# Optimization experiments

Measured on AMD Instinct MI355X. Metric: run time of the kernel, lower is better.

Reference implementation:

```python
import jax, jax.numpy as jnp
import numpy as np
from jax import lax

B, C, IMG, PATCH = 128, 3, 224, 16
EMB, HEADS = 384, 6
NPATCH = (IMG // PATCH) ** 2          # 196
NTOK = NPATCH + 1                     # 197 (cls token)
HID = int(EMB * 4.0)                  # 1536 (also expert hidden)
NE, K = 4, 2                          # num_experts (hardcoded 4), top-k
NCLS = 1000


def _ln(x, g, b, eps=1e-5):
    m = jnp.mean(x, axis=-1, keepdims=True)
    v = jnp.mean((x - m) ** 2, axis=-1, keepdims=True)
    return (x - m) * lax.rsqrt(v + eps) * g + b


def setup_inputs() -> dict:
    key = jax.random.key(0)
    ks = jax.random.split(key, 16)
    s = 0.02
    return {
        "x": jax.random.normal(ks[0], (B, C, IMG, IMG), jnp.float32),
        "conv_w": jax.random.normal(ks[1], (EMB, C, PATCH, PATCH), jnp.float32) * s,
        "conv_b": jnp.zeros((EMB,), jnp.float32),
        "cls_token": jax.random.normal(ks[2], (1, 1, EMB), jnp.float32) * s,
        "pos_embed": jax.random.normal(ks[3], (1, NTOK, EMB), jnp.float32) * s,
        "ln1_g": jnp.ones((EMB,), jnp.float32),
        "ln1_b": jnp.zeros((EMB,), jnp.float32),
        "in_proj_w": jax.random.normal(ks[4], (3 * EMB, EMB), jnp.float32) * s,
        "in_proj_b": jnp.zeros((3 * EMB,), jnp.float32),
        "out_proj_w": jax.random.normal(ks[5], (EMB, EMB), jnp.float32) * s,
        "out_proj_b": jnp.zeros((EMB,), jnp.float32),
        "router_w": jax.random.normal(ks[6], (NE, EMB), jnp.float32) * s,
        "router_b": jnp.zeros((NE,), jnp.float32),
        "ew1": jax.random.normal(ks[7], (NE, EMB, HID), jnp.float32) * s,
        "eb1": jnp.zeros((NE, HID), jnp.float32),
        "ew2": jax.random.normal(ks[8], (NE, HID, EMB), jnp.float32) * s,
        "eb2": jnp.zeros((NE, EMB), jnp.float32),
        "ln2_g": jnp.ones((EMB,), jnp.float32),
        "ln2_b": jnp.zeros((EMB,), jnp.float32),
        "head_w": jax.random.normal(ks[9], (NCLS, EMB), jnp.float32) * s,
        "head_b": jnp.zeros((NCLS,), jnp.float32),
    }


def reference(x, conv_w, conv_b, cls_token, pos_embed,
              ln1_g, ln1_b, in_proj_w, in_proj_b, out_proj_w, out_proj_b,
              router_w, router_b, ew1, eb1, ew2, eb2,
              ln2_g, ln2_b, head_w, head_b):
    # ---- patch embedding: Conv2d(stride=kernel=patch) -> [B, N, E]
    h = lax.conv_general_dilated(x, conv_w, window_strides=(PATCH, PATCH),
                                 padding="VALID",
                                 dimension_numbers=("NCHW", "OIHW", "NCHW"))
    h = h + conv_b[None, :, None, None]
    h = h.reshape(B, EMB, NPATCH).transpose(0, 2, 1)          # [B, 196, E]
    h = jnp.concatenate([jnp.broadcast_to(cls_token, (B, 1, EMB)), h], axis=1)
    h = h + pos_embed                                         # [B, 197, E]

    # ---- SelfAttentionBlock (NOTE: no residual; same LN applied twice, as in source)
    hn = _ln(h, ln1_g, ln1_b)
    qkv = hn @ in_proj_w.T + in_proj_b                        # [B, N, 3E]
    q, k, v = jnp.split(qkv, 3, axis=-1)
    hd = EMB // HEADS
    q = q.reshape(B, NTOK, HEADS, hd)
    k = k.reshape(B, NTOK, HEADS, hd)
    v = v.reshape(B, NTOK, HEADS, hd)
    att = jnp.einsum("bqhd,bkhd->bhqk", q, k) / np.sqrt(hd).astype(np.float32)
    att = jax.nn.softmax(att, axis=-1)
    o = jnp.einsum("bhqk,bkhd->bqhd", att, v).reshape(B, NTOK, EMB)
    o = o @ out_proj_w.T + out_proj_b
    h = _ln(o, ln1_g, ln1_b)                                  # second LN, same params

    # ---- MoE: dense all-expert FFN + top-k gather + mean
    scores = jax.nn.softmax(h @ router_w.T + router_b, axis=-1)   # [B, N, NE]
    topk_vals, topk_idx = lax.top_k(scores, K)                    # [B, N, K]
    flat = h.reshape(B * NTOK, EMB)
    eh = jax.nn.gelu(jnp.einsum("te,neh->tnh", flat, ew1) + eb1, approximate=False)
    eo = jnp.einsum("tnh,nhe->tne", eh, ew2) + eb2                # [BN, NE, E]
    idx = topk_idx.reshape(B * NTOK, K, 1)
    sel = jnp.take_along_axis(eo, idx, axis=1)                    # [BN, K, E]
    h = sel.mean(axis=1).reshape(B, NTOK, EMB)

    # ---- final norm + classification head on cls token
    h = _ln(h, ln2_g, ln2_b)
    return h[:, 0] @ head_w.T + head_b                            # [B, NCLS]
```

## Files before the change

kernel.cpp:

```cpp
#include <hip/hip_runtime.h>
#include <cstdint>
#include <cstddef>

typedef _Float16 f16;
typedef _Float16 f16x2 __attribute__((ext_vector_type(2)));
typedef _Float16 f16x8 __attribute__((ext_vector_type(8)));
typedef float    f32x4 __attribute__((ext_vector_type(4)));

constexpr int NTOKC  = 197;
constexpr int TTOK   = 128 * 197;
constexpr int EMB    = 384;
constexpr int HID    = 1536;

constexpr size_t OFF_CONVW   = 0;
constexpr size_t OFF_EW1T    = 1179648;
constexpr size_t OFF_EW2T    = 5898240;
constexpr size_t OFF_HEADW16 = 10616832;
constexpr size_t OFF_XCLS16  = 11403264;
constexpr size_t OFF_Q       = 11404800;
constexpr size_t OFF_HCLS16  = 11799552;
constexpr size_t OFF_MASKW   = 11897856;
constexpr size_t OFF_EH      = 11899904;
constexpr size_t OFF_EPART   = 13472768;
constexpr size_t OFF_HFIN    = 16618496;
constexpr size_t OFF_XH      = 16716800;
constexpr size_t OFF_R       = 36082688;
constexpr size_t OFF_CVEC    = 36094976;
constexpr size_t OFF_U16     = 36099072;
constexpr size_t OFF_O16     = 36688896;
constexpr size_t OFF_WV16    = 36787200;
constexpr size_t OFF_WOUT16  = 37082112;
constexpr size_t OFF_O2CLS   = 37377024;
constexpr size_t OFF_P32     = 37573632;
constexpr size_t OFF_SG      = 38212608;
constexpr size_t OFF_SCLS    = 38817792;
constexpr size_t WS_NEEDED   = 38818816;

__device__ __forceinline__ void gload16(const void* g, void* l) {
  __builtin_amdgcn_global_load_lds(
      (__attribute__((address_space(1))) void*)(void*)g,
      (__attribute__((address_space(3))) void*)l, 16, 0, 0);
}

__global__ __launch_bounds__(256) void prep_cast_k(
    const float* __restrict__ conv_w, const float* __restrict__ head_w,
    const float* __restrict__ inp_w, const float* __restrict__ outp_w,
    f16* __restrict__ convw, f16* __restrict__ headw16,
    f16* __restrict__ wv16, f16* __restrict__ wout16) {
  int i = blockIdx.x * 256 + threadIdx.x;
  if (i < 294912) convw[i] = (f16)conv_w[i];
  int j = i - 294912;
  if (j >= 0 && j < 393216) {
    int row = j / 384;
    headw16[j] = (row < 1000) ? (f16)head_w[j] : (f16)0.f;
  }
  int k = i - 688128;
  if (k >= 0 && k < 147456) wv16[k] = (f16)inp_w[294912 + k];
  int l = i - 835584;
  if (l >= 0 && l < 147456) wout16[l] = (f16)outp_w[l];
}

__global__ __launch_bounds__(256) void transpose_cast_k(
    const float* __restrict__ in, f16* __restrict__ outp, int R, int C) {
  __shared__ float tile[32][33];
  int e = blockIdx.z;
  const float* pin = in + (size_t)e * R * C;
  f16* pout = outp + (size_t)e * R * C;
  int c0 = blockIdx.x * 32, r0 = blockIdx.y * 32;
  int tx = threadIdx.x & 31, ty = threadIdx.x >> 5;
#pragma unroll
  for (int i = 0; i < 4; i++)
    tile[ty + 8 * i][tx] = pin[(size_t)(r0 + ty + 8 * i) * C + c0 + tx];
  __syncthreads();
#pragma unroll
  for (int i = 0; i < 4; i++)
    pout[(size_t)(c0 + ty + 8 * i) * R + r0 + tx] = (f16)tile[tx][ty + 8 * i];
}

__global__ __launch_bounds__(384) void clsprep_k(
    const float* __restrict__ cls, const float* __restrict__ posw,
    const float* __restrict__ g, const float* __restrict__ bb,
    const float* __restrict__ Wq, const float* __restrict__ bq,
    f16* __restrict__ xcls16, float* __restrict__ qout) {
  __shared__ float xs[EMB];
  __shared__ float red[16];
  int t = threadIdx.x, lane = t & 63, wave = t >> 6;
  float v = cls[t] + posw[t];
  float s = v, sq = v * v;
#pragma unroll
  for (int off = 32; off; off >>= 1) {
    s += __shfl_xor(s, off);
    sq += __shfl_xor(sq, off);
  }
  if (lane == 0) { red[wave] = s; red[8 + wave] = sq; }
  __syncthreads();
  float S = 0.f, SQ = 0.f;
#pragma unroll
  for (int i = 0; i < 6; i++) { S += red[i]; SQ += red[8 + i]; }
  float m = S * (1.f / 384.f);
  float rs = rsqrtf(SQ * (1.f / 384.f) - m * m + 1e-5f);
  float y = (v - m) * rs * g[t] + bb[t];
  xs[t] = y;
  xcls16[t] = (f16)y;
  __syncthreads();
  const float4* w4 = (const float4*)(Wq + (size_t)t * EMB);
  const float4* s4 = (const float4*)xs;
  float a = bq[t];
#pragma unroll 8
  for (int i = 0; i < 96; i++) {
    float4 xx = s4[i], ww = w4[i];
    a += xx.x * ww.x + xx.y * ww.y + xx.z * ww.z + xx.w * ww.w;
  }
  qout[t] = a;
}

__global__ __launch_bounds__(384) void rprep_k(
    const float* __restrict__ inp_w, const float* __restrict__ inp_b,
    const float* __restrict__ qv, const f16* __restrict__ xcls16,
    float* __restrict__ Rg, float* __restrict__ Cg, float* __restrict__ Scls) {
  int h = blockIdx.x, t = threadIdx.x;
  __shared__ float qs[64];
  __shared__ float cred[64];
  __shared__ float sred[6];
  if (t < 64) {
    float q = qv[h * 64 + t];
    qs[t] = q;
    cred[t] = q * inp_b[384 + h * 64 + t];
  }
  __syncthreads();
  const float* wp = inp_w + ((size_t)(384 + h * 64)) * 384 + t;
  float a = 0.f;
#pragma unroll 8
  for (int d = 0; d < 64; d++) a += wp[(size_t)d * 384] * qs[d];
  Rg[h * 384 + t] = a;
  float part = a * (float)xcls16[t];
  int lane = t & 63, wave = t >> 6;
#pragma unroll
  for (int off = 32; off; off >>= 1) part += __shfl_xor(part, off);
  if (lane == 0) sred[wave] = part;
  __syncthreads();
  if (t == 0) {
    float c = 0.f;
    for (int d = 0; d < 64; d++) c += cred[d];
    Cg[h] = c;
    float stot = c;
#pragma unroll
    for (int i = 0; i < 6; i++) stot += sred[i];
    Scls[h] = stot;
  }
}

__global__ __launch_bounds__(384) void bcast_cls_k(
    const f16* __restrict__ xcls16, const float* __restrict__ Scls,
    f16* __restrict__ xh, float* __restrict__ Sg) {
  int b = blockIdx.x, t = threadIdx.x;
  xh[(size_t)b * NTOKC * EMB + t] = xcls16[t];
  if (t < 6) Sg[((size_t)b * 6 + t) * 197] = Scls[t];
}

__global__ __launch_bounds__(1024) void embed_ln_k(
    const float* __restrict__ img, const f16* __restrict__ B,
    const float* __restrict__ bias, const float* __restrict__ posw,
    const float* __restrict__ g, const float* __restrict__ bb,
    const float* __restrict__ Rg, const float* __restrict__ Cg,
    f16* __restrict__ xh, float* __restrict__ Sg) {
  __shared__ __attribute__((aligned(16))) char smem[57344];
  f16* As0 = (f16*)smem;
  f16* As1 = (f16*)(smem + 4096);
  f16* Bs0 = (f16*)(smem + 8192);
  f16* Bs1 = (f16*)(smem + 32768);
  const int K = 768;
  const int NT = 24;
  const int tid = threadIdx.x;
  const int lane = tid & 63;
  const int wave = tid >> 6;
  const int rowgrp = wave & 3;
  const int colgrp = wave >> 2;
  const int m0 = (int)blockIdx.x * 64;
  const int fr = lane & 15;
  const int fq = lane >> 4;

  f32x4 acc[6];
#pragma unroll
  for (int j = 0; j < 6; j++) acc[j] = f32x4{0.f, 0.f, 0.f, 0.f};

  const int sr = lane >> 2, sc = (lane & 3) * 8;
  const float* abase = nullptr;
  int adoff = 0;
  if (wave < 4) {
    int row = m0 + wave * 16 + sr;
    int bimg = row / 196;
    int pp = row - bimg * 196;
    int py = pp / 14, px = pp - py * 14;
    int kx0 = sc & 15;
    abase = img + ((size_t)(bimg * 3) * 224 + py * 16) * 224 + px * 16 + kx0;
    adoff = (wave * 16 + sr) * 32 + sc;
  }
  const f16* gb0 = nullptr;
  int lboff = 0;
  if (wave >= 4) {
    int brow = (wave - 4) * 32;
    gb0 = B + (size_t)(brow + sr) * K + sc;
    lboff = brow * 32;
  }

  float4 n0, n1;
  if (wave < 4) {
    {
      int col = sc;
      const float* src = abase + (col >> 8) * 50176 + ((col >> 4) & 15) * 224;
      float4 p0 = *(const float4*)src;
      float4 p1 = *(const float4*)(src + 4);
      f16x8 hv;
      hv[0] = (f16)p0.x; hv[1] = (f16)p0.y; hv[2] = (f16)p0.z; hv[3] = (f16)p0.w;
      hv[4] = (f16)p1.x; hv[5] = (f16)p1.y; hv[6] = (f16)p1.z; hv[7] = (f16)p1.w;
      *(f16x8*)(As0 + adoff) = hv;
    }
    {
      int col = 32 + sc;
      const float* src = abase + (col >> 8) * 50176 + ((col >> 4) & 15) * 224;
      n0 = *(const float4*)src;
      n1 = *(const float4*)(src + 4);
    }
  } else {
    gload16(gb0, Bs0 + lboff);
    gload16(gb0 + (size_t)16 * K, Bs0 + lboff + 16 * 32);
    gb0 += 32;
  }
  __syncthreads();

  f16* AsC = As0; f16* AsN = As1;
  f16* BsC = Bs0; f16* BsN = Bs1;

  for (int t = 0; t < NT; ++t) {
    if (wave < 4) {
      if (t + 1 < NT) {
        f16x8 hv;
        hv[0] = (f16)n0.x; hv[1] = (f16)n0.y; hv[2] = (f16)n0.z; hv[3] = (f16)n0.w;
        hv[4] = (f16)n1.x; hv[5] = (f16)n1.y; hv[6] = (f16)n1.z; hv[7] = (f16)n1.w;
        *(f16x8*)(AsN + adoff) = hv;
      }
      if (t + 2 < NT) {
        int col = (t + 2) * 32 + sc;
        const float* src = abase + (col >> 8) * 50176 + ((col >> 4) & 15) * 224;
        n0 = *(const float4*)src;
        n1 = *(const float4*)(src + 4);
      }
    } else {
      if (t + 1 < NT) {
        gload16(gb0, BsN + lboff);
        gload16(gb0 + (size_t)16 * K, BsN + lboff + 16 * 32);
        gb0 += 32;
      }
    }
    f16x8 af = *(const f16x8*)&AsC[(rowgrp * 16 + fr) * 32 + fq * 8];
#pragma unroll
    for (int j = 0; j < 6; j++) {
      f16x8 bf = *(const f16x8*)&BsC[(colgrp * 96 + j * 16 + fr) * 32 + fq * 8];
      acc[j] = __builtin_amdgcn_mfma_f32_16x16x32_f16(af, bf, acc[j], 0, 0, 0);
    }
    __syncthreads();
    f16* tA = AsC; AsC = AsN; AsN = tA;
    f16* tB = BsC; BsC = BsN; BsN = tB;
  }

  float* prm   = (float*)smem;
  float* psum  = (float*)(smem + 4608);
  float* pqsum = (float*)(smem + 5632);
  float* Rs2   = (float*)(smem + 6656);
  float* psc   = (float*)(smem + 15872);
  for (int i = tid; i < 1152; i += 1024)
    prm[i] = (i < 384) ? bias[i] : ((i < 768) ? g[i - 384] : bb[i - 768]);
  for (int i = tid; i < 2304; i += 1024) Rs2[i] = Rg[i];
  __syncthreads();

  float v[4][6];
#pragma unroll
  for (int rg = 0; rg < 4; rg++) {
    int lrow = rowgrp * 16 + fq * 4 + rg;
    int row = m0 + lrow;
    int bimg = row / 196;
    int pp = row - bimg * 196;
    const float* prow = posw + (size_t)(pp + 1) * EMB;
    float s = 0.f, sq = 0.f;
#pragma unroll
    for (int j = 0; j < 6; j++) {
      int col = colgrp * 96 + j * 16 + fr;
      float t = acc[j][rg] + prm[col] + prow[col];
      v[rg][j] = t;
      s += t; sq += t * t;
    }
#pragma unroll
    for (int off = 1; off < 16; off <<= 1) {
      s += __shfl_xor(s, off);
      sq += __shfl_xor(sq, off);
    }
    if (fr == 0) { psum[lrow * 4 + colgrp] = s; pqsum[lrow * 4 + colgrp] = sq; }
  }
  __syncthreads();

#pragma unroll
  for (int rg = 0; rg < 4; rg++) {
    int lrow = rowgrp * 16 + fq * 4 + rg;
    float S = psum[lrow * 4] + psum[lrow * 4 + 1] + psum[lrow * 4 + 2] + psum[lrow * 4 + 3];
    float SQ = pqsum[lrow * 4] + pqsum[lrow * 4 + 1] + pqsum[lrow * 4 + 2] + pqsum[lrow * 4 + 3];
    float m = S * (1.f / 384.f);
    float rs = rsqrtf(SQ * (1.f / 384.f) - m * m + 1e-5f);
    int row = m0 + lrow;
    int bimg = row / 196;
    int pp = row - bimg * 196;
    f16* orow = xh + ((size_t)bimg * NTOKC + pp + 1) * EMB;
#pragma unroll
    for (int j = 0; j < 6; j++) {
      int col = colgrp * 96 + j * 16 + fr;
      float y = (v[rg][j] - m) * rs * prm[384 + col] + prm[768 + col];
      v[rg][j] = y;
      orow[col] = (f16)y;
    }
  }

#pragma unroll
  for (int h = 0; h < 6; h++) {
    float rv[6];
#pragma unroll
    for (int j = 0; j < 6; j++)
      rv[j] = Rs2[h * 384 + colgrp * 96 + j * 16 + fr];
#pragma unroll
    for (int rg = 0; rg < 4; rg++) {
      float p = v[rg][0] * rv[0] + v[rg][1] * rv[1] + v[rg][2] * rv[2]
              + v[rg][3] * rv[3] + v[rg][4] * rv[4] + v[rg][5] * rv[5];
#pragma unroll
      for (int off = 1; off < 16; off <<= 1) p += __shfl_xor(p, off);
      if (fr == 0) psc[(rowgrp * 16 + fq * 4 + rg) * 24 + colgrp * 6 + h] = p;
    }
  }
  __syncthreads();
  if (tid < 384) {
    int lrow = tid / 6, h = tid - lrow * 6;
    float s = psc[lrow * 24 + h] + psc[lrow * 24 + 6 + h]
            + psc[lrow * 24 + 12 + h] + psc[lrow * 24 + 18 + h] + Cg[h];
    int row = m0 + lrow;
    int bimg = row / 196, pp = row - bimg * 196;
    Sg[((size_t)bimg * 6 + h) * 197 + pp + 1] = s;
  }
}

__global__ __launch_bounds__(384) void softmax_k(
    const float* __restrict__ Sg, float* __restrict__ P32) {
  const int b = blockIdx.x, tid = threadIdx.x;
  const int wave = tid >> 6, lane = tid & 63;
  const float* sp = Sg + ((size_t)b * 6 + wave) * 197;
  float z[4], pk[4];
#pragma unroll
  for (int k = 0; k < 4; k++) {
    int t = lane + 64 * k;
    z[k] = (t < 197) ? sp[t] * 0.125f : -1e30f;
    pk[k] = 0.f;
  }
  float mx = fmaxf(fmaxf(z[0], z[1]), fmaxf(z[2], z[3]));
#pragma unroll
  for (int off = 32; off; off >>= 1) mx = fmaxf(mx, __shfl_xor(mx, off));
  float sum = 0.f;
#pragma unroll
  for (int k = 0; k < 4; k++) {
    int t = lane + 64 * k;
    if (t < 197) {
      pk[k] = __expf(z[k] - mx);
      sum += pk[k];
    }
  }
#pragma unroll
  for (int off = 32; off; off >>= 1) sum += __shfl_xor(sum, off);
  float si = 1.f / sum;
#pragma unroll
  for (int k = 0; k < 4; k++) {
    int t = lane + 64 * k;
    if (t < 208) P32[(size_t)b * 1248 + wave * 208 + t] = pk[k] * si;
  }
}

__global__ __launch_bounds__(256) void u_gemv_k(
    const float* __restrict__ P32, const f16* __restrict__ xh,
    f16* __restrict__ U16) {
  __shared__ float pf[6 * 208];
  __shared__ float part[4][64][12];
  const int cq = (int)blockIdx.x;
  const int b  = (int)blockIdx.y;
  const int tid = threadIdx.x;
  for (int i = tid; i < 1248; i += 256) pf[i] = P32[(size_t)b * 1248 + i];
  __syncthreads();
  const int cp = tid & 63;
  const int tq = tid >> 6;
  const int col0 = cq * 128 + cp * 2;
  const int t0 = 49 * tq;
  const int t1 = (tq == 3) ? 197 : t0 + 49;
  float acc[12];
#pragma unroll
  for (int r = 0; r < 12; r++) acc[r] = 0.f;
  const f16* xp = xh + ((size_t)b * NTOKC + t0) * EMB + col0;
#pragma unroll 2
  for (int t = t0; t < t1; t++) {
    f16x2 xv = *(const f16x2*)xp;
    float x0 = (float)xv[0];
    float x1 = (float)xv[1];
    xp += EMB;
#pragma unroll
    for (int h = 0; h < 6; h++) {
      float p = pf[h * 208 + t];
      acc[h * 2]     += p * x0;
      acc[h * 2 + 1] += p * x1;
    }
  }
#pragma unroll
  for (int r = 0; r < 12; r++) part[tq][cp][r] = acc[r];
  __syncthreads();
#pragma unroll
  for (int k = 0; k < 3; k++) {
    int idx = tid + k * 256;
    int cp2 = idx / 12, slot = idx - cp2 * 12;
    int h = slot >> 1, c01 = slot & 1;
    float u = part[0][cp2][slot] + part[1][cp2][slot] +
              part[2][cp2][slot] + part[3][cp2][slot];
    U16[(size_t)b * 2304 + h * 384 + cq * 128 + cp2 * 2 + c01] = (f16)u;
  }
}

__global__ __launch_bounds__(256) void vproj_k(
    const f16* __restrict__ U16, const f16* __restrict__ wv16,
    const float* __restrict__ inp_b, f16* __restrict__ O16) {
  __shared__ f16 As[128 * 32];
  __shared__ f16 Bs[64 * 32];
  const int tid = threadIdx.x;
  const int lane = tid & 63;
  const int wave = tid >> 6;
  const int h = (int)blockIdx.x;
  const int wm = (wave >> 1) * 64;
  const int wn = (wave & 1) * 32;
  const int fr = lane & 15;
  const int fq = lane >> 4;
  const float* bv = inp_b + 768 + h * 64;

  f32x4 acc[4][2];
#pragma unroll
  for (int i = 0; i < 4; i++)
#pragma unroll
    for (int j = 0; j < 2; j++) acc[i][j] = f32x4{0.f, 0.f, 0.f, 0.f};

  const int sr = lane >> 2;
  const int sc = (lane & 3) * 8;
  const f16* ag = U16 + (size_t)(wave * 32 + sr) * 2304 + h * 384 + sc;
  const f16* bg = wv16 + (size_t)(h * 64 + wave * 16 + sr) * 384 + sc;
  const size_t rstepA = (size_t)16 * 2304;
  f16* la = As + wave * 32 * 32;
  f16* lb = Bs + wave * 16 * 32;

  for (int k0 = 0; k0 < 384; k0 += 32) {
    gload16(ag, la);  gload16(ag + rstepA, la + 16 * 32);
    gload16(bg, lb);
    ag += 32; bg += 32;
    __syncthreads();
    f16x8 af[4], bf[2];
#pragma unroll
    for (int i = 0; i < 4; i++)
      af[i] = *(const f16x8*)&As[(wm + i * 16 + fr) * 32 + fq * 8];
#pragma unroll
    for (int j = 0; j < 2; j++)
      bf[j] = *(const f16x8*)&Bs[(wn + j * 16 + fr) * 32 + fq * 8];
#pragma unroll
    for (int i = 0; i < 4; i++)
#pragma unroll
      for (int j = 0; j < 2; j++)
        acc[i][j] = __builtin_amdgcn_mfma_f32_16x16x32_f16(af[i], bf[j], acc[i][j], 0, 0, 0);
    __syncthreads();
  }

#pragma unroll
  for (int i = 0; i < 4; i++)
#pragma unroll
    for (int j = 0; j < 2; j++)
#pragma unroll
      for (int rg = 0; rg < 4; rg++) {
        int gm = wm + i * 16 + fq * 4 + rg;
        int gn = wn + j * 16 + fr;
        O16[(size_t)gm * EMB + h * 64 + gn] = (f16)(acc[i][j][rg] + bv[gn]);
      }
}

__global__ __launch_bounds__(256) void oproj_k(
    const f16* __restrict__ O16, const f16* __restrict__ wout16,
    const float* __restrict__ bout, float* __restrict__ o2cls) {
  __shared__ f16 As[128 * 32];
  __shared__ f16 Bs[64 * 32];
  const int tid = threadIdx.x;
  const int lane = tid & 63;
  const int wave = tid >> 6;
  const int n0 = (int)blockIdx.x * 64;
  const int wm = (wave >> 1) * 64;
  const int wn = (wave & 1) * 32;
  const int fr = lane & 15;
  const int fq = lane >> 4;

  f32x4 acc[4][2];
#pragma unroll
  for (int i = 0; i < 4; i++)
#pragma unroll
    for (int j = 0; j < 2; j++) acc[i][j] = f32x4{0.f, 0.f, 0.f, 0.f};

  const int sr = lane >> 2;
  const int sc = (lane & 3) * 8;
  const f16* ag = O16 + (size_t)(wave * 32 + sr) * 384 + sc;
  const f16* bg = wout16 + (size_t)(n0 + wave * 16 + sr) * 384 + sc;
  const size_t rstep = (size_t)16 * 384;
  f16* la = As + wave * 32 * 32;
  f16* lb = Bs + wave * 16 * 32;

  for (int k0 = 0; k0 < 384; k0 += 32) {
    gload16(ag, la);  gload16(ag + rstep, la + 16 * 32);
    gload16(bg, lb);
    ag += 32; bg += 32;
    __syncthreads();
    f16x8 af[4], bf[2];
#pragma unroll
    for (int i = 0; i < 4; i++)
      af[i] = *(const f16x8*)&As[(wm + i * 16 + fr) * 32 + fq * 8];
#pragma unroll
    for (int j = 0; j < 2; j++)
      bf[j] = *(const f16x8*)&Bs[(wn + j * 16 + fr) * 32 + fq * 8];
#pragma unroll
    for (int i = 0; i < 4; i++)
#pragma unroll
      for (int j = 0; j < 2; j++)
        acc[i][j] = __builtin_amdgcn_mfma_f32_16x16x32_f16(af[i], bf[j], acc[i][j], 0, 0, 0);
    __syncthreads();
  }

#pragma unroll
  for (int i = 0; i < 4; i++)
#pragma unroll
    for (int j = 0; j < 2; j++)
#pragma unroll
      for (int rg = 0; rg < 4; rg++) {
        int gm = wm + i * 16 + fq * 4 + rg;
        int gn = n0 + wn + j * 16 + fr;
        o2cls[(size_t)gm * EMB + gn] = acc[i][j][rg] + bout[gn];
      }
}

__global__ __launch_bounds__(384) void ln_router_k(
    const float* __restrict__ o2cls, const float* __restrict__ g, const float* __restrict__ bb,
    const float* __restrict__ rw, const float* __restrict__ rb,
    f16* __restrict__ hcls16, float* __restrict__ maskw) {
  __shared__ float red[16];
  __shared__ float part[6][4];
  __shared__ float logits[4];
  int b = blockIdx.x, t = threadIdx.x;
  int lane = t & 63, wave = t >> 6;
  float v = o2cls[(size_t)b * EMB + t];
  float s = v, sq = v * v;
#pragma unroll
  for (int off = 32; off; off >>= 1) {
    s += __shfl_xor(s, off);
    sq += __shfl_xor(sq, off);
  }
  if (lane == 0) { red[wave] = s; red[8 + wave] = sq; }
  __syncthreads();
  float S = 0.f, SQ = 0.f;
#pragma unroll
  for (int i = 0; i < 6; i++) { S += red[i]; SQ += red[8 + i]; }
  float m = S * (1.f / 384.f);
  float rs = rsqrtf(SQ * (1.f / 384.f) - m * m + 1e-5f);
  float y = (v - m) * rs * g[t] + bb[t];
  hcls16[(size_t)b * EMB + t] = (f16)y;
  float p0 = y * rw[t];
  float p1 = y * rw[EMB + t];
  float p2 = y * rw[2 * EMB + t];
  float p3 = y * rw[3 * EMB + t];
#pragma unroll
  for (int off = 32; off; off >>= 1) {
    p0 += __shfl_xor(p0, off);
    p1 += __shfl_xor(p1, off);
    p2 += __shfl_xor(p2, off);
    p3 += __shfl_xor(p3, off);
  }
  if (lane == 0) { part[wave][0] = p0; part[wave][1] = p1; part[wave][2] = p2; part[wave][3] = p3; }
  __syncthreads();
  if (t < 4) {
    float a = rb[t];
#pragma unroll
    for (int i = 0; i < 6; i++) a += part[i][t];
    logits[t] = a;
  }
  __syncthreads();
  if (t == 0) {
    float l0 = logits[0], l1 = logits[1], l2 = logits[2], l3 = logits[3];
    int i1 = 0; float b1 = l0;
    if (l1 > b1) { b1 = l1; i1 = 1; }
    if (l2 > b1) { b1 = l2; i1 = 2; }
    if (l3 > b1) { b1 = l3; i1 = 3; }
    int i2 = -1; float b2 = 0.f;
    float lv[4] = {l0, l1, l2, l3};
#pragma unroll
    for (int i = 0; i < 4; i++) {
      if (i == i1) continue;
      if (i2 < 0 || lv[i] > b2) { i2 = i; b2 = lv[i]; }
    }
#pragma unroll
    for (int e = 0; e < 4; e++)
      maskw[(size_t)b * 4 + e] = (e == i1 || e == i2) ? 0.5f : 0.f;
  }
}

__global__ __launch_bounds__(256) void moe1_k(
    const f16* __restrict__ A, const f16* __restrict__ Bm,
    const float* __restrict__ bias, f16* __restrict__ outh) {
  __shared__ f16 As[128 * 32];
  __shared__ f16 Bs[64 * 32];
  const int K = EMB;
  const int tid = threadIdx.x;
  const int lane = tid & 63;
  const int wave = tid >> 6;
  const int e = (int)blockIdx.y;
  const int n0 = (int)blockIdx.x * 64;
  const int wm = (wave >> 1) * 64;
  const int wn = (wave & 1) * 32;
  const int fr = lane & 15;
  const int fq = lane >> 4;
  Bm += (size_t)e * HID * EMB;
  bias += (size_t)e * HID;

  f32x4 acc[4][2];
#pragma unroll
  for (int i = 0; i < 4; i++)
#pragma unroll
    for (int j = 0; j < 2; j++) acc[i][j] = f32x4{0.f, 0.f, 0.f, 0.f};

  const int sr = lane >> 2;
  const int sc = (lane & 3) * 8;
  const f16* ag = A + (size_t)(wave * 32 + sr) * K + sc;
  const f16* bg = Bm + (size_t)(n0 + wave * 16 + sr) * K + sc;
  const size_t rstep = (size_t)16 * K;
// ... 145 lines not shown
  const int wn = (wave & 1) * 64;
  const int fr = lane & 15;
  const int fq = lane >> 4;

  f32x4 acc[4][4];
#pragma unroll
  for (int i = 0; i < 4; i++)
#pragma unroll
    for (int j = 0; j < 4; j++) acc[i][j] = f32x4{0.f, 0.f, 0.f, 0.f};

  const int srow = wave * 32 + (lane >> 2);
  const int scol = (lane & 3) * 8;
  const f16* ag = A + (size_t)srow * K + scol;
  const f16* bg = B + (size_t)(n0 + srow) * K + scol;
  const size_t rstep = (size_t)16 * K;
  f16* la = As + wave * 32 * 32;
  f16* lb = Bs + wave * 32 * 32;

  for (int k0 = 0; k0 < K; k0 += 32) {
    gload16(ag, la);          gload16(ag + rstep, la + 16 * 32);
    gload16(bg, lb);          gload16(bg + rstep, lb + 16 * 32);
    ag += 32; bg += 32;
    __syncthreads();
    f16x8 af[4], bf[4];
#pragma unroll
    for (int i = 0; i < 4; i++) {
      af[i] = *(const f16x8*)&As[(wm + i * 16 + fr) * 32 + fq * 8];
      bf[i] = *(const f16x8*)&Bs[(wn + i * 16 + fr) * 32 + fq * 8];
    }
#pragma unroll
    for (int i = 0; i < 4; i++)
#pragma unroll
      for (int j = 0; j < 4; j++)
        acc[i][j] = __builtin_amdgcn_mfma_f32_16x16x32_f16(af[i], bf[j], acc[i][j], 0, 0, 0);
    __syncthreads();
  }

#pragma unroll
  for (int i = 0; i < 4; i++)
#pragma unroll
    for (int j = 0; j < 4; j++)
#pragma unroll
      for (int rg = 0; rg < 4; rg++) {
        int gm = wm + i * 16 + fq * 4 + rg;
        int gn = n0 + wn + j * 16 + fr;
        if (gn < 1000)
          outp[(size_t)gm * 1000 + gn] = acc[i][j][rg] + hb[gn];
      }
}

extern "C" void kernel_launch(void* const* d_in, const int* in_sizes, int n_in,
                              void* d_out, int out_size, void* d_ws, size_t ws_size,
                              hipStream_t stream) {
  const float* x      = (const float*)d_in[0];
  const float* conv_w = (const float*)d_in[1];
  const float* conv_b = (const float*)d_in[2];
  const float* cls_t  = (const float*)d_in[3];
  const float* pos    = (const float*)d_in[4];
  const float* ln1_g  = (const float*)d_in[5];
  const float* ln1_b  = (const float*)d_in[6];
  const float* inp_w  = (const float*)d_in[7];
  const float* inp_b  = (const float*)d_in[8];
  const float* outp_w = (const float*)d_in[9];
  const float* outp_b = (const float*)d_in[10];
  const float* rt_w   = (const float*)d_in[11];
  const float* rt_b   = (const float*)d_in[12];
  const float* ew1    = (const float*)d_in[13];
  const float* eb1    = (const float*)d_in[14];
  const float* ew2    = (const float*)d_in[15];
  const float* eb2    = (const float*)d_in[16];
  const float* ln2_g  = (const float*)d_in[17];
  const float* ln2_b  = (const float*)d_in[18];
  const float* head_w = (const float*)d_in[19];
  const float* head_b = (const float*)d_in[20];
  float* out = (float*)d_out;
  char* w = (char*)d_ws;
  if (ws_size < WS_NEEDED) return;

  f16* convw    = (f16*)(w + OFF_CONVW);
  f16* ew1t     = (f16*)(w + OFF_EW1T);
  f16* ew2t     = (f16*)(w + OFF_EW2T);
  f16* headw16  = (f16*)(w + OFF_HEADW16);
  f16* xcls16   = (f16*)(w + OFF_XCLS16);
  float* qvec   = (float*)(w + OFF_Q);
  f16* hcls16   = (f16*)(w + OFF_HCLS16);
  float* maskw  = (float*)(w + OFF_MASKW);
  f16* ehbuf    = (f16*)(w + OFF_EH);
  float* epart  = (float*)(w + OFF_EPART);
  f16* hfin     = (f16*)(w + OFF_HFIN);
  f16* xh       = (f16*)(w + OFF_XH);
  float* Rg     = (float*)(w + OFF_R);
  float* Cg     = (float*)(w + OFF_CVEC);
  f16* u16      = (f16*)(w + OFF_U16);
  f16* o16      = (f16*)(w + OFF_O16);
  f16* wv16     = (f16*)(w + OFF_WV16);
  f16* wout16   = (f16*)(w + OFF_WOUT16);
  float* o2cls  = (float*)(w + OFF_O2CLS);
  float* p32    = (float*)(w + OFF_P32);
  float* sg     = (float*)(w + OFF_SG);
  float* scls   = (float*)(w + OFF_SCLS);

  prep_cast_k<<<dim3(3840), 256, 0, stream>>>(
      conv_w, head_w, inp_w, outp_w, convw, headw16, wv16, wout16);
  transpose_cast_k<<<dim3(48, 12, 4), 256, 0, stream>>>(ew1, ew1t, 384, 1536);
  transpose_cast_k<<<dim3(12, 48, 4), 256, 0, stream>>>(ew2, ew2t, 1536, 384);

  clsprep_k<<<dim3(1), 384, 0, stream>>>(cls_t, pos, ln1_g, ln1_b, inp_w, inp_b, xcls16, qvec);
  rprep_k<<<dim3(6), 384, 0, stream>>>(inp_w, inp_b, qvec, xcls16, Rg, Cg, scls);
  bcast_cls_k<<<dim3(128), 384, 0, stream>>>(xcls16, scls, xh, sg);

  embed_ln_k<<<dim3(392), 1024, 0, stream>>>(
      x, convw, conv_b, pos, ln1_g, ln1_b, Rg, Cg, xh, sg);

  softmax_k<<<dim3(128), 384, 0, stream>>>(sg, p32);
  u_gemv_k<<<dim3(3, 128), 256, 0, stream>>>(p32, xh, u16);
  vproj_k<<<dim3(6), 256, 0, stream>>>(u16, wv16, inp_b, o16);
  oproj_k<<<dim3(6), 256, 0, stream>>>(o16, wout16, outp_b, o2cls);
  ln_router_k<<<dim3(128), 384, 0, stream>>>(
      o2cls, ln1_g, ln1_b, rt_w, rt_b, hcls16, maskw);

  moe1_k<<<dim3(24, 4), 256, 0, stream>>>(hcls16, ew1t, eb1, ehbuf);
  moe2_k<<<dim3(6, 4, 4), 256, 0, stream>>>(ehbuf, ew2t, epart);
  combine_ln2_k<<<dim3(128), 384, 0, stream>>>(epart, eb2, maskw, ln2_g, ln2_b, hfin);

  head_gemm_k<<<dim3(8), 256, 0, stream>>>(hfin, headw16, head_b, out);
  (void)in_sizes; (void)n_in; (void)out_size;
}
```

Baseline: 321.7 us.

## Fold V and output projections into one weight, merge prep kernels, swizzle LDS

Precomputes a fused matrix F = Wout·Wv per head, plus a combined bias, in a single merged prep kernel, so the V projection and output projection collapse into one split-K GEMM whose partial sums are reduced inside the LN/router kernel. The separate prep, transpose, cls-prep, broadcast and softmax kernels are folded into fewer launches, with softmax moved into u_gemv and the cls broadcast into embed_ln. The embedding GEMM gains an XOR-swizzled LDS layout and a deeper A-prefetch. This cuts launch count and intermediate buffers, at the cost of a larger fused-weight GEMM with a K of 2304 and extra prep work to build F.

```diff
diff --git a/kernel.cpp b/kernel.cpp
--- a/kernel.cpp
+++ b/kernel.cpp
@@ -17,7 +17,6 @@
 constexpr size_t OFF_EW2T    = 5898240;
 constexpr size_t OFF_HEADW16 = 10616832;
 constexpr size_t OFF_XCLS16  = 11403264;
-constexpr size_t OFF_Q       = 11404800;
 constexpr size_t OFF_HCLS16  = 11799552;
 constexpr size_t OFF_MASKW   = 11897856;
 constexpr size_t OFF_EH      = 11899904;
@@ -27,14 +26,12 @@
 constexpr size_t OFF_R       = 36082688;
 constexpr size_t OFF_CVEC    = 36094976;
 constexpr size_t OFF_U16     = 36099072;
-constexpr size_t OFF_O16     = 36688896;
-constexpr size_t OFF_WV16    = 36787200;
-constexpr size_t OFF_WOUT16  = 37082112;
-constexpr size_t OFF_O2CLS   = 37377024;
-constexpr size_t OFF_P32     = 37573632;
 constexpr size_t OFF_SG      = 38212608;
 constexpr size_t OFF_SCLS    = 38817792;
-constexpr size_t WS_NEEDED   = 38818816;
+constexpr size_t OFF_F       = 38818816;
+constexpr size_t OFF_B2      = 40588288;
+constexpr size_t OFF_FPART   = 40589824;
+constexpr size_t WS_NEEDED   = 41179648;
 
 __device__ __forceinline__ void gload16(const void* g, void* l) {
   __builtin_amdgcn_global_load_lds(
@@ -42,49 +39,101 @@
       (__attribute__((address_space(3))) void*)l, 16, 0, 0);
 }
 
-__global__ __launch_bounds__(256) void prep_cast_k(
+#define PACK8(hv, p0, p1) { hv[0]=(f16)p0.x; hv[1]=(f16)p0.y; hv[2]=(f16)p0.z; hv[3]=(f16)p0.w; \
+                            hv[4]=(f16)p1.x; hv[5]=(f16)p1.y; hv[6]=(f16)p1.z; hv[7]=(f16)p1.w; }
+
+__global__ __launch_bounds__(256) void prep_all_k(
     const float* __restrict__ conv_w, const float* __restrict__ head_w,
-    const float* __restrict__ inp_w, const float* __restrict__ outp_w,
+    const float* __restrict__ ew1, const float* __restrict__ ew2,
+    const float* __restrict__ inp_w, const float* __restrict__ inp_b,
+    const float* __restrict__ outp_w, const float* __restrict__ outp_b,
     f16* __restrict__ convw, f16* __restrict__ headw16,
-    f16* __restrict__ wv16, f16* __restrict__ wout16) {
-  int i = blockIdx.x * 256 + threadIdx.x;
-  if (i < 294912) convw[i] = (f16)conv_w[i];
-  int j = i - 294912;
-  if (j >= 0 && j < 393216) {
-    int row = j / 384;
-    headw16[j] = (row < 1000) ? (f16)head_w[j] : (f16)0.f;
-  }
-  int k = i - 688128;
-  if (k >= 0 && k < 147456) wv16[k] = (f16)inp_w[294912 + k];
-  int l = i - 835584;
-  if (l >= 0 && l < 147456) wout16[l] = (f16)outp_w[l];
-}
-
-__global__ __launch_bounds__(256) void transpose_cast_k(
-    const float* __restrict__ in, f16* __restrict__ outp, int R, int C) {
-  __shared__ float tile[32][33];
-  int e = blockIdx.z;
-  const float* pin = in + (size_t)e * R * C;
-  f16* pout = outp + (size_t)e * R * C;
-  int c0 = blockIdx.x * 32, r0 = blockIdx.y * 32;
-  int tx = threadIdx.x & 31, ty = threadIdx.x >> 5;
-#pragma unroll
-  for (int i = 0; i < 4; i++)
-    tile[ty + 8 * i][tx] = pin[(size_t)(r0 + ty + 8 * i) * C + c0 + tx];
-  __syncthreads();
-#pragma unroll
-  for (int i = 0; i < 4; i++)
-    pout[(size_t)(c0 + ty + 8 * i) * R + r0 + tx] = (f16)tile[tx][ty + 8 * i];
-}
-
-__global__ __launch_bounds__(384) void clsprep_k(
+    f16* __restrict__ ew1t, f16* __restrict__ ew2t,
+    f16* __restrict__ F, float* __restrict__ bias2) {
+  __shared__ __attribute__((aligned(16))) char sbuf[4352];
+  const int bx = (int)blockIdx.x, tid = threadIdx.x;
+  if (bx < 2688) {
+    int i = bx * 256 + tid;
+    if (i < 294912) convw[i] = (f16)conv_w[i];
+    int j = i - 294912;
+    if (j >= 0 && j < 393216) {
+      int row = j / 384;
+      headw16[j] = (row < 1000) ? (f16)head_w[j] : (f16)0.f;
+    }
+  } else if (bx < 4992) {
+    float (*tile)[33] = (float(*)[33])sbuf;
+    int local = bx - 2688;
+    int e = local / 576, r2 = local - e * 576;
+    int byy = r2 / 48, bxx = r2 - byy * 48;
+    const float* pin = ew1 + (size_t)e * 384 * 1536;
+    f16* pout = ew1t + (size_t)e * 384 * 1536;
+    int c0 = bxx * 32, r0 = byy * 32;
+    int tx = tid & 31, ty = tid >> 5;
+#pragma unroll
+    for (int i = 0; i < 4; i++)
+      tile[ty + 8 * i][tx] = pin[(size_t)(r0 + ty + 8 * i) * 1536 + c0 + tx];
+    __syncthreads();
+#pragma unroll
+    for (int i = 0; i < 4; i++)
+      pout[(size_t)(c0 + ty + 8 * i) * 384 + r0 + tx] = (f16)tile[tx][ty + 8 * i];
+  } else if (bx < 7296) {
+    float (*tile)[33] = (float(*)[33])sbuf;
+    int local = bx - 4992;
+    int e = local / 576, r2 = local - e * 576;
+    int byy = r2 / 12, bxx = r2 - byy * 12;
+    const float* pin = ew2 + (size_t)e * 1536 * 384;
+    f16* pout = ew2t + (size_t)e * 1536 * 384;
+    int c0 = bxx * 32, r0 = byy * 32;
+    int tx = tid & 31, ty = tid >> 5;
+#pragma unroll
+    for (int i = 0; i < 4; i++)
+      tile[ty + 8 * i][tx] = pin[(size_t)(r0 + ty + 8 * i) * 384 + c0 + tx];
+    __syncthreads();
+#pragma unroll
+    for (int i = 0; i < 4; i++)
+      pout[(size_t)(c0 + ty + 8 * i) * 1536 + r0 + tx] = (f16)tile[tx][ty + 8 * i];
+  } else if (bx < 7440) {
+    float (*wo)[64] = (float(*)[64])sbuf;
+    int local = bx - 7296;
+    int h = local / 24, nt = local - h * 24;
+    int n0 = nt * 16;
+    for (int i = tid; i < 1024; i += 256) {
+      int ni = i >> 6, d = i & 63;
+      wo[ni][d] = outp_w[(size_t)(n0 + ni) * 384 + h * 64 + d];
+    }
+    __syncthreads();
+    for (int e = tid; e < 6144; e += 256) {
+      int ni = e / 384, k2 = e - ni * 384;
+      const float* wv = inp_w + (size_t)(768 + h * 64) * 384 + k2;
+      float a = 0.f;
+#pragma unroll 8
+      for (int d = 0; d < 64; d++) a += wo[ni][d] * wv[(size_t)d * 384];
+      F[(size_t)(n0 + ni) * 2304 + h * 384 + k2] = (f16)a;
+    }
+  } else {
+    int nt = bx - 7440;
+    if (tid < 16) {
+      int n = nt * 16 + tid;
+      const float* wrow = outp_w + (size_t)n * 384;
+      float a = outp_b[n];
+      for (int c = 0; c < 384; c++) a += wrow[c] * inp_b[768 + c];
+      bias2[n] = a;
+    }
+  }
+}
+
+__global__ __launch_bounds__(384) void clsrprep_k(
     const float* __restrict__ cls, const float* __restrict__ posw,
     const float* __restrict__ g, const float* __restrict__ bb,
-    const float* __restrict__ Wq, const float* __restrict__ bq,
-    f16* __restrict__ xcls16, float* __restrict__ qout) {
+    const float* __restrict__ inp_w, const float* __restrict__ inp_b,
+    f16* __restrict__ xcls16, float* __restrict__ Rg,
+    float* __restrict__ Cg, float* __restrict__ Scls) {
   __shared__ float xs[EMB];
   __shared__ float red[16];
-  int t = threadIdx.x, lane = t & 63, wave = t >> 6;
+  __shared__ float qh[64];
+  __shared__ float sred[6];
+  const int h = (int)blockIdx.x, t = threadIdx.x;
+  const int lane = t & 63, wave = t >> 6;
   float v = cls[t] + posw[t];
   float s = v, sq = v * v;
 #pragma unroll
@@ -103,66 +152,41 @@
   xs[t] = y;
   xcls16[t] = (f16)y;
   __syncthreads();
-  const float4* w4 = (const float4*)(Wq + (size_t)t * EMB);
-  const float4* s4 = (const float4*)xs;
-  float a = bq[t];
+  if (t < 64) {
+    const float* wq = inp_w + (size_t)(h * 64 + t) * 384;
+    float a = inp_b[h * 64 + t];
 #pragma unroll 8
-  for (int i = 0; i < 96; i++) {
-    float4 xx = s4[i], ww = w4[i];
-    a += xx.x * ww.x + xx.y * ww.y + xx.z * ww.z + xx.w * ww.w;
-  }
-  qout[t] = a;
-}
-
-__global__ __launch_bounds__(384) void rprep_k(
-    const float* __restrict__ inp_w, const float* __restrict__ inp_b,
-    const float* __restrict__ qv, const f16* __restrict__ xcls16,
-    float* __restrict__ Rg, float* __restrict__ Cg, float* __restrict__ Scls) {
-  int h = blockIdx.x, t = threadIdx.x;
-  __shared__ float qs[64];
-  __shared__ float cred[64];
-  __shared__ float sred[6];
-  if (t < 64) {
-    float q = qv[h * 64 + t];
-    qs[t] = q;
-    cred[t] = q * inp_b[384 + h * 64 + t];
-  }
-  __syncthreads();
-  const float* wp = inp_w + ((size_t)(384 + h * 64)) * 384 + t;
+    for (int c = 0; c < 384; c++) a += wq[c] * xs[c];
+    qh[t] = a;
+  }
+  __syncthreads();
+  const float* wp = inp_w + (size_t)(384 + h * 64) * 384 + t;
   float a = 0.f;
 #pragma unroll 8
-  for (int d = 0; d < 64; d++) a += wp[(size_t)d * 384] * qs[d];
+  for (int d = 0; d < 64; d++) a += wp[(size_t)d * 384] * qh[d];
   Rg[h * 384 + t] = a;
-  float part = a * (float)xcls16[t];
-  int lane = t & 63, wave = t >> 6;
+  float part = a * xs[t];
 #pragma unroll
   for (int off = 32; off; off >>= 1) part += __shfl_xor(part, off);
   if (lane == 0) sred[wave] = part;
   __syncthreads();
   if (t == 0) {
     float c = 0.f;
-    for (int d = 0; d < 64; d++) c += cred[d];
+    for (int d = 0; d < 64; d++) c += qh[d] * inp_b[384 + h * 64 + d];
     Cg[h] = c;
-    float stot = c;
-#pragma unroll
-    for (int i = 0; i < 6; i++) stot += sred[i];
-    Scls[h] = stot;
-  }
-}
-
-__global__ __launch_bounds__(384) void bcast_cls_k(
-    const f16* __restrict__ xcls16, const float* __restrict__ Scls,
-    f16* __restrict__ xh, float* __restrict__ Sg) {
-  int b = blockIdx.x, t = threadIdx.x;
-  xh[(size_t)b * NTOKC * EMB + t] = xcls16[t];
-  if (t < 6) Sg[((size_t)b * 6 + t) * 197] = Scls[t];
-}
-
-__global__ __launch_bounds__(1024) void embed_ln_k(
+    float st = c;
+#pragma unroll
+    for (int i = 0; i < 6; i++) st += sred[i];
+    Scls[h] = st;
+  }
+}
+
+__global__ __launch_bounds__(1024, 8) void embed_ln_k(
     const float* __restrict__ img, const f16* __restrict__ B,
     const float* __restrict__ bias, const float* __restrict__ posw,
     const float* __restrict__ g, const float* __restrict__ bb,
     const float* __restrict__ Rg, const float* __restrict__ Cg,
+    const f16* __restrict__ xcls16, const float* __restrict__ Scls,
     f16* __restrict__ xh, float* __restrict__ Sg) {
   __shared__ __attribute__((aligned(16))) char smem[57344];
   f16* As0 = (f16*)smem;
@@ -180,11 +204,19 @@
   const int fr = lane & 15;
   const int fq = lane >> 4;
 
+  if (blockIdx.x < 128) {
+    if (tid < 384) xh[(size_t)blockIdx.x * NTOKC * EMB + tid] = xcls16[tid];
+    if (tid < 6) Sg[((size_t)blockIdx.x * 6 + tid) * 197] = Scls[tid];
+  }
+
   f32x4 acc[6];
 #pragma unroll
   for (int j = 0; j < 6; j++) acc[j] = f32x4{0.f, 0.f, 0.f, 0.f};
 
   const int sr = lane >> 2, sc = (lane & 3) * 8;
+  const int swzS = (((lane & 3) ^ (sr & 3)) * 8);
+  const int swzR = ((fq ^ (fr & 3)) * 8);
+
   const float* abase = nullptr;
   int adoff = 0;
   if (wave < 4) {
@@ -194,33 +226,35 @@
     int py = pp / 14, px = pp - py * 14;
     int kx0 = sc & 15;
     abase = img + ((size_t)(bimg * 3) * 224 + py * 16) * 224 + px * 16 + kx0;
-    adoff = (wave * 16 + sr) * 32 + sc;
+    adoff = (wave * 16 + sr) * 32 + swzS;
   }
   const f16* gb0 = nullptr;
   int lboff = 0;
   if (wave >= 4) {
     int brow = (wave - 4) * 32;
-    gb0 = B + (size_t)(brow + sr) * K + sc;
+    gb0 = B + (size_t)(brow + sr) * K + swzS;
     lboff = brow * 32;
   }
 
-  float4 n0, n1;
+  float4 a0x, a0y, a1x, a1y;
   if (wave < 4) {
     {
       int col = sc;
       const float* src = abase + (col >> 8) * 50176 + ((col >> 4) & 15) * 224;
       float4 p0 = *(const float4*)src;
       float4 p1 = *(const float4*)(src + 4);
-      f16x8 hv;
-      hv[0] = (f16)p0.x; hv[1] = (f16)p0.y; hv[2] = (f16)p0.z; hv[3] = (f16)p0.w;
-      hv[4] = (f16)p1.x; hv[5] = (f16)p1.y; hv[6] = (f16)p1.z; hv[7] = (f16)p1.w;
+      f16x8 hv; PACK8(hv, p0, p1);
       *(f16x8*)(As0 + adoff) = hv;
     }
     {
       int col = 32 + sc;
       const float* src = abase + (col >> 8) * 50176 + ((col >> 4) & 15) * 224;
-      n0 = *(const float4*)src;
-      n1 = *(const float4*)(src + 4);
+      a0x = *(const float4*)src; a0y = *(const float4*)(src + 4);
+    }
+    {
+      int col = 64 + sc;
+      const float* src = abase + (col >> 8) * 50176 + ((col >> 4) & 15) * 224;
+      a1x = *(const float4*)src; a1y = *(const float4*)(src + 4);
     }
   } else {
     gload16(gb0, Bs0 + lboff);
@@ -236,15 +270,15 @@
     if (wave < 4) {
       if (t + 1 < NT) {
         f16x8 hv;
-        hv[0] = (f16)n0.x; hv[1] = (f16)n0.y; hv[2] = (f16)n0.z; hv[3] = (f16)n0.w;
-        hv[4] = (f16)n1.x; hv[5] = (f16)n1.y; hv[6] = (f16)n1.z; hv[7] = (f16)n1.w;
+        if ((t & 1) == 0) { PACK8(hv, a0x, a0y); }
+        else              { PACK8(hv, a1x, a1y); }
         *(f16x8*)(AsN + adoff) = hv;
       }
-      if (t + 2 < NT) {
-        int col = (t + 2) * 32 + sc;
+      if (t + 3 < NT) {
+        int col = (t + 3) * 32 + sc;
         const float* src = abase + (col >> 8) * 50176 + ((col >> 4) & 15) * 224;
-        n0 = *(const float4*)src;
-        n1 = *(const float4*)(src + 4);
+        if ((t & 1) == 0) { a0x = *(const float4*)src; a0y = *(const float4*)(src + 4); }
+        else              { a1x = *(const float4*)src; a1y = *(const float4*)(src + 4); }
       }
     } else {
       if (t + 1 < NT) {
@@ -253,10 +287,10 @@
         gb0 += 32;
       }
     }
-    f16x8 af = *(const f16x8*)&AsC[(rowgrp * 16 + fr) * 32 + fq * 8];
+    f16x8 af = *(const f16x8*)&AsC[(rowgrp * 16 + fr) * 32 + swzR];
 #pragma unroll
     for (int j = 0; j < 6; j++) {
-      f16x8 bf = *(const f16x8*)&BsC[(colgrp * 96 + j * 16 + fr) * 32 + fq * 8];
+      f16x8 bf = *(const f16x8*)&BsC[(colgrp * 96 + j * 16 + fr) * 32 + swzR];
       acc[j] = __builtin_amdgcn_mfma_f32_16x16x32_f16(af, bf, acc[j], 0, 0, 0);
     }
     __syncthreads();
@@ -345,50 +379,48 @@
   }
 }
 
-__global__ __launch_bounds__(384) void softmax_k(
-    const float* __restrict__ Sg, float* __restrict__ P32) {
-  const int b = blockIdx.x, tid = threadIdx.x;
-  const int wave = tid >> 6, lane = tid & 63;
-  const float* sp = Sg + ((size_t)b * 6 + wave) * 197;
-  float z[4], pk[4];
-#pragma unroll
-  for (int k = 0; k < 4; k++) {
-    int t = lane + 64 * k;
-    z[k] = (t < 197) ? sp[t] * 0.125f : -1e30f;
-    pk[k] = 0.f;
-  }
-  float mx = fmaxf(fmaxf(z[0], z[1]), fmaxf(z[2], z[3]));
-#pragma unroll
-  for (int off = 32; off; off >>= 1) mx = fmaxf(mx, __shfl_xor(mx, off));
-  float sum = 0.f;
-#pragma unroll
-  for (int k = 0; k < 4; k++) {
-    int t = lane + 64 * k;
-    if (t < 197) {
-      pk[k] = __expf(z[k] - mx);
-      sum += pk[k];
-    }
-  }
-#pragma unroll
-  for (int off = 32; off; off >>= 1) sum += __shfl_xor(sum, off);
-  float si = 1.f / sum;
-#pragma unroll
-  for (int k = 0; k < 4; k++) {
-    int t = lane + 64 * k;
-    if (t < 208) P32[(size_t)b * 1248 + wave * 208 + t] = pk[k] * si;
-  }
-}
-
 __global__ __launch_bounds__(256) void u_gemv_k(
-    const float* __restrict__ P32, const f16* __restrict__ xh,
+    const float* __restrict__ Sg, const f16* __restrict__ xh,
     f16* __restrict__ U16) {
   __shared__ float pf[6 * 208];
   __shared__ float part[4][64][12];
   const int cq = (int)blockIdx.x;
   const int b  = (int)blockIdx.y;
   const int tid = threadIdx.x;
-  for (int i = tid; i < 1248; i += 256) pf[i] = P32[(size_t)b * 1248 + i];
-  __syncthreads();
+  const int wave = tid >> 6, lane = tid & 63;
+
+  for (int h = wave; h < 6; h += 4) {
+    const float* sp = Sg + ((size_t)b * 6 + h) * 197;
+    float z[4], pk[4];
+#pragma unroll
+    for (int k = 0; k < 4; k++) {
+      int t = lane + 64 * k;
+      z[k] = (t < 197) ? sp[t] * 0.125f : -1e30f;
+      pk[k] = 0.f;
+    }
+    float mx = fmaxf(fmaxf(z[0], z[1]), fmaxf(z[2], z[3]));
+#pragma unroll
+    for (int off = 32; off; off >>= 1) mx = fmaxf(mx, __shfl_xor(mx, off));
+    float sum = 0.f;
+#pragma unroll
+    for (int k = 0; k < 4; k++) {
+      int t = lane + 64 * k;
+      if (t < 197) {
+        pk[k] = __expf(z[k] - mx);
+        sum += pk[k];
+      }
+    }
+#pragma unroll
+    for (int off = 32; off; off >>= 1) sum += __shfl_xor(sum, off);
+    float si = 1.f / sum;
+#pragma unroll
+    for (int k = 0; k < 4; k++) {
+      int t = lane + 64 * k;
+      if (t < 208) pf[h * 208 + t] = pk[k] * si;
+    }
+  }
+  __syncthreads();
+
   const int cp = tid & 63;
   const int tq = tid >> 6;
   const int col0 = cq * 128 + cp * 2;
@@ -425,76 +457,16 @@
   }
 }
 
-__global__ __launch_bounds__(256) void vproj_k(
-    const f16* __restrict__ U16, const f16* __restrict__ wv16,
-    const float* __restrict__ inp_b, f16* __restrict__ O16) {
-  __shared__ f16 As[128 * 32];
-  __shared__ f16 Bs[64 * 32];
-  const int tid = threadIdx.x;
-  const int lane = tid & 63;
-  const int wave = tid >> 6;
-  const int h = (int)blockIdx.x;
-  const int wm = (wave >> 1) * 64;
-  const int wn = (wave & 1) * 32;
-  const int fr = lane & 15;
-  const int fq = lane >> 4;
-  const float* bv = inp_b + 768 + h * 64;
-
-  f32x4 acc[4][2];
-#pragma unroll
-  for (int i = 0; i < 4; i++)
-#pragma unroll
-    for (int j = 0; j < 2; j++) acc[i][j] = f32x4{0.f, 0.f, 0.f, 0.f};
-
-  const int sr = lane >> 2;
-  const int sc = (lane & 3) * 8;
-  const f16* ag = U16 + (size_t)(wave * 32 + sr) * 2304 + h * 384 + sc;
-  const f16* bg = wv16 + (size_t)(h * 64 + wave * 16 + sr) * 384 + sc;
-  const size_t rstepA = (size_t)16 * 2304;
-  f16* la = As + wave * 32 * 32;
-  f16* lb = Bs + wave * 16 * 32;
-
-  for (int k0 = 0; k0 < 384; k0 += 32) {
-    gload16(ag, la);  gload16(ag + rstepA, la + 16 * 32);
-    gload16(bg, lb);
-    ag += 32; bg += 32;
-    __syncthreads();
-    f16x8 af[4], bf[2];
-#pragma unroll
-    for (int i = 0; i < 4; i++)
-      af[i] = *(const f16x8*)&As[(wm + i * 16 + fr) * 32 + fq * 8];
-#pragma unroll
-    for (int j = 0; j < 2; j++)
-      bf[j] = *(const f16x8*)&Bs[(wn + j * 16 + fr) * 32 + fq * 8];
-#pragma unroll
-    for (int i = 0; i < 4; i++)
-#pragma unroll
-      for (int j = 0; j < 2; j++)
-        acc[i][j] = __builtin_amdgcn_mfma_f32_16x16x32_f16(af[i], bf[j], acc[i][j], 0, 0, 0);
-    __syncthreads();
-  }
-
-#pragma unroll
-  for (int i = 0; i < 4; i++)
-#pragma unroll
-    for (int j = 0; j < 2; j++)
-#pragma unroll
-      for (int rg = 0; rg < 4; rg++) {
-        int gm = wm + i * 16 + fq * 4 + rg;
-        int gn = wn + j * 16 + fr;
-        O16[(size_t)gm * EMB + h * 64 + gn] = (f16)(acc[i][j][rg] + bv[gn]);
-      }
-}
-
-__global__ __launch_bounds__(256) void oproj_k(
-    const f16* __restrict__ O16, const f16* __restrict__ wout16,
-    const float* __restrict__ bout, float* __restrict__ o2cls) {
+__global__ __launch_bounds__(256) void fproj_k(
+    const f16* __restrict__ U16, const f16* __restrict__ F,
+    float* __restrict__ fpart) {
   __shared__ f16 As[128 * 32];
   __shared__ f16 Bs[64 * 32];
   const int tid = threadIdx.x;
   const int lane = tid & 63;
   const int wave = tid >> 6;
   const int n0 = (int)blockIdx.x * 64;
+  const int kc = (int)blockIdx.y;
   const int wm = (wave >> 1) * 64;
   const int wn = (wave & 1) * 32;
   const int fr = lane & 15;
@@ -508,13 +480,13 @@
 
   const int sr = lane >> 2;
   const int sc = (lane & 3) * 8;
-  const f16* ag = O16 + (size_t)(wave * 32 + sr) * 384 + sc;
-  const f16* bg = wout16 + (size_t)(n0 + wave * 16 + sr) * 384 + sc;
-  const size_t rstep = (size_t)16 * 384;
+  const f16* ag = U16 + (size_t)(wave * 32 + sr) * 2304 + kc * 768 + sc;
+  const f16* bg = F + (size_t)(n0 + wave * 16 + sr) * 2304 + kc * 768 + sc;
+  const size_t rstep = (size_t)16 * 2304;
   f16* la = As + wave * 32 * 32;
   f16* lb = Bs + wave * 16 * 32;
 
-  for (int k0 = 0; k0 < 384; k0 += 32) {
+  for (int k0 = 0; k0 < 768; k0 += 32) {
     gload16(ag, la);  gload16(ag + rstep, la + 16 * 32);
     gload16(bg, lb);
     ag += 32; bg += 32;
@@ -542,12 +514,13 @@
       for (int rg = 0; rg < 4; rg++) {
         int gm = wm + i * 16 + fq * 4 + rg;
         int gn = n0 + wn + j * 16 + fr;
-        o2cls[(size_t)gm * EMB + gn] = acc[i][j][rg] + bout[gn];
+        fpart[((size_t)kc * 128 + gm) * EMB + gn] = acc[i][j][rg];
       }
 }
 
 __global__ __launch_bounds__(384) void ln_router_k(
-    const float* __restrict__ o2cls, const float* __restrict__ g, const float* __restrict__ bb,
+    const float* __restrict__ fpart, const float* __restrict__ bias2,
+    const float* __restrict__ g, const float* __restrict__ bb,
     const float* __restrict__ rw, const float* __restrict__ rb,
     f16* __restrict__ hcls16, float* __restrict__ maskw) {
   __shared__ float red[16];
@@ -555,7 +528,9 @@
   __shared__ float logits[4];
   int b = blockIdx.x, t = threadIdx.x;
   int lane = t & 63, wave = t >> 6;
-  float v = o2cls[(size_t)b * EMB + t];
+  float v = fpart[(size_t)b * EMB + t]
+          + fpart[((size_t)128 + b) * EMB + t]
+          + fpart[((size_t)256 + b) * EMB + t] + bias2[t];
   float s = v, sq = v * v;
 #pragma unroll
   for (int off = 32; off; off >>= 1) {
@@ -867,7 +842,6 @@
   f16* ew2t     = (f16*)(w + OFF_EW2T);
   f16* headw16  = (f16*)(w + OFF_HEADW16);
   f16* xcls16   = (f16*)(w + OFF_XCLS16);
-  float* qvec   = (float*)(w + OFF_Q);
   f16* hcls16   = (f16*)(w + OFF_HCLS16);
   float* maskw  = (float*)(w + OFF_MASKW);
   f16* ehbuf    = (f16*)(w + OFF_EH);
@@ -877,32 +851,27 @@
   float* Rg     = (float*)(w + OFF_R);
   float* Cg     = (float*)(w + OFF_CVEC);
   f16* u16      = (f16*)(w + OFF_U16);
-  f16* o16      = (f16*)(w + OFF_O16);
-  f16* wv16     = (f16*)(w + OFF_WV16);
-  f16* wout16   = (f16*)(w + OFF_WOUT16);
-  float* o2cls  = (float*)(w + OFF_O2CLS);
-  float* p32    = (float*)(w + OFF_P32);
   float* sg     = (float*)(w + OFF_SG);
   float* scls   = (float*)(w + OFF_SCLS);
-
-  prep_cast_k<<<dim3(3840), 256, 0, stream>>>(
-      conv_w, head_w, inp_w, outp_w, convw, headw16, wv16, wout16);
-  transpose_cast_k<<<dim3(48, 12, 4), 256, 0, stream>>>(ew1, ew1t, 384, 1536);
-  transpose_cast_k<<<dim3(12, 48, 4), 256, 0, stream>>>(ew2, ew2t, 1536, 384);
-
-  clsprep_k<<<dim3(1), 384, 0, stream>>>(cls_t, pos, ln1_g, ln1_b, inp_w, inp_b, xcls16, qvec);
-  rprep_k<<<dim3(6), 384, 0, stream>>>(inp_w, inp_b, qvec, xcls16, Rg, Cg, scls);
-  bcast_cls_k<<<dim3(128), 384, 0, stream>>>(xcls16, scls, xh, sg);
+  f16* Fw       = (f16*)(w + OFF_F);
+  float* bias2  = (float*)(w + OFF_B2);
+  float* fpart  = (float*)(w + OFF_FPART);
+
+  prep_all_k<<<dim3(7464), 256, 0, stream>>>(
+      conv_w, head_w, ew1, ew2, inp_w, inp_b, outp_w, outp_b,
+      convw, headw16, ew1t, ew2t, Fw, bias2);
+
+  clsrprep_k<<<dim3(6), 384, 0, stream>>>(
+      cls_t, pos, ln1_g, ln1_b, inp_w, inp_b, xcls16, Rg, Cg, scls);
 
   embed_ln_k<<<dim3(392), 1024, 0, stream>>>(
-      x, convw, conv_b, pos, ln1_g, ln1_b, Rg, Cg, xh, sg);
-
-  softmax_k<<<dim3(128), 384, 0, stream>>>(sg, p32);
-  u_gemv_k<<<dim3(3, 128), 256, 0, stream>>>(p32, xh, u16);
-  vproj_k<<<dim3(6), 256, 0, stream>>>(u16, wv16, inp_b, o16);
-  oproj_k<<<dim3(6), 256, 0, stream>>>(o16, wout16, outp_b, o2cls);
+      x, convw, conv_b, pos, ln1_g, ln1_b, Rg, Cg, xcls16, scls, xh, sg);
+
+  u_gemv_k<<<dim3(3, 128), 256, 0, stream>>>(sg, xh, u16);
+
+  fproj_k<<<dim3(6, 3), 256, 0, stream>>>(u16, Fw, fpart);
   ln_router_k<<<dim3(128), 384, 0, stream>>>(
-      o2cls, ln1_g, ln1_b, rt_w, rt_b, hcls16, maskw);
+      fpart, bias2, ln1_g, ln1_b, rt_w, rt_b, hcls16, maskw);
 
   moe1_k<<<dim3(24, 4), 256, 0, stream>>>(hcls16, ew1t, eb1, ehbuf);
   moe2_k<<<dim3(6, 4, 4), 256, 0, stream>>>(ehbuf, ew2t, epart);
```

Result: slower. 365.6 us (+13.7%).
